# Kernel tuning notes

Hardware: AMD Instinct MI355X
Metric: run time of the kernel (lower is better)

## Reference

```python
import jax, jax.numpy as jnp
import numpy as np

NEG_SLOPE = 0.2
EPS = 1e-16


def gat_conv(x, edge_index, W, a_src, a_dst, b, heads, out_c, concat):
    # PyG GATConv: lin (no bias) -> per-head attention logits -> self-loops ->
    # leaky_relu -> softmax over incoming edges per dst -> weighted scatter-add -> bias
    N = x.shape[0]
    loop = jnp.arange(N)
    src = jnp.concatenate([edge_index[0], loop])  # [E+N]
    dst = jnp.concatenate([edge_index[1], loop])
    h = (x @ W).reshape(N, heads, out_c)                    # [N,H,C]
    a_s = jnp.sum(h * a_src[None], axis=-1)                 # [N,H]
    a_d = jnp.sum(h * a_dst[None], axis=-1)                 # [N,H]
    e = jax.nn.leaky_relu(a_s[src] + a_d[dst], NEG_SLOPE)   # [E+N,H]
    m = jax.ops.segment_max(e, dst, num_segments=N)         # stable softmax per dst
    e = jnp.exp(e - m[dst])
    s = jax.ops.segment_sum(e, dst, num_segments=N)
    alpha = e / (s[dst] + EPS)                              # [E+N,H]
    msg = h[src] * alpha[:, :, None]                        # [E+N,H,C]
    out = jax.ops.segment_sum(msg, dst, num_segments=N)     # [N,H,C]
    out = out.reshape(N, heads * out_c) if concat else out.mean(axis=1)
    return out + b


def setup_inputs() -> dict:
    key = jax.random.key(0)
    ks = jax.random.split(key, 20)
    N, E = 50000, 800000
    IN, HID, H, OUT = 128, 32, 4, 1
    HC = H * HID  # 128
    g = lambda k, shp: jax.random.normal(k, shp, dtype=jnp.float32) * 0.05
    inp = {
        "x": jax.random.normal(ks[0], (N, IN), dtype=jnp.float32),
        "edge_index": jax.random.randint(ks[1], (2, E), 0, N, dtype=jnp.int64),
        "batch": jnp.zeros((N,), dtype=jnp.int64),
        # conv0: GATConv(128 -> 32, heads=4, concat)
        "c0_w": g(ks[2], (IN, HC)), "c0_asrc": g(ks[3], (H, HID)),
        "c0_adst": g(ks[4], (H, HID)), "c0_b": jnp.zeros((HC,), jnp.float32),
        "s0_w": g(ks[5], (HC, IN)), "s0_b": jnp.zeros((HC,), jnp.float32),
        # conv1: GATConv(128 -> 32, heads=4, concat)
        "c1_w": g(ks[6], (HC, HC)), "c1_asrc": g(ks[7], (H, HID)),
        "c1_adst": g(ks[8], (H, HID)), "c1_b": jnp.zeros((HC,), jnp.float32),
        "s1_w": g(ks[9], (HC, HC)), "s1_b": jnp.zeros((HC,), jnp.float32),
        # conv2: GATConv(128 -> 1, heads=1, concat=False)
        "c2_w": g(ks[10], (HC, OUT)), "c2_asrc": g(ks[11], (1, OUT)),
        "c2_adst": g(ks[12], (1, OUT)), "c2_b": jnp.zeros((OUT,), jnp.float32),
        "s2_w": g(ks[13], (OUT, HC)), "s2_b": jnp.zeros((OUT,), jnp.float32),
    }
    return inp


def reference(x, edge_index, batch,
              c0_w, c0_asrc, c0_adst, c0_b, s0_w, s0_b,
              c1_w, c1_asrc, c1_adst, c1_b, s1_w, s1_b,
              c2_w, c2_asrc, c2_adst, c2_b, s2_w, s2_b):
    # layer 0 (dropout is identity in eval mode)
    h = jax.nn.relu(gat_conv(x, edge_index, c0_w, c0_asrc, c0_adst, c0_b, 4, 32, True)
                    + x @ s0_w.T + s0_b)
    # layer 1
    h = jax.nn.relu(gat_conv(h, edge_index, c1_w, c1_asrc, c1_adst, c1_b, 4, 32, True)
                    + h @ s1_w.T + s1_b)
    # output layer: heads=1, concat=False (mean over heads)
    h = (gat_conv(h, edge_index, c2_w, c2_asrc, c2_adst, c2_b, 1, 1, False)
         + h @ s2_w.T + s2_b)
    return jax.nn.sigmoid(h)
```

## Files before the change

### kernel.cpp

```cpp
#include <hip/hip_runtime.h>
#include <math.h>

#define TPB 256

typedef short bf16x8 __attribute__((ext_vector_type(8)));
typedef float f32x4 __attribute__((ext_vector_type(4)));

static __device__ __forceinline__ float lrelu(float x) { return x > 0.f ? x : 0.2f * x; }
static __device__ __forceinline__ unsigned short f2bf(float f) {
  unsigned u = __float_as_uint(f);
  u += 0x7fffu + ((u >> 16) & 1u);
  return (unsigned short)(u >> 16);
}
static __device__ __forceinline__ float bflo(unsigned w) { return __uint_as_float(w << 16); }
static __device__ __forceinline__ float bfhi(unsigned w) { return __uint_as_float(w & 0xffff0000u); }

__global__ void k_hist(const int* __restrict__ dstE, int E, int N, int* __restrict__ deg) {
  int e = blockIdx.x * TPB + threadIdx.x;
  if (e >= E + N) return;
  int d = (e < E) ? dstE[e] : (e - E);
  d = min(max(d, 0), N - 1);
  atomicAdd(&deg[d], 1);
}

__global__ void k_scan1(const int* __restrict__ deg, int N, int* __restrict__ csum) {
  __shared__ int sm[TPB];
  int t = threadIdx.x, i = blockIdx.x * TPB + t;
  sm[t] = (i < N) ? deg[i] : 0;
  __syncthreads();
  for (int off = TPB / 2; off; off >>= 1) {
    if (t < off) sm[t] += sm[t + off];
    __syncthreads();
  }
  if (t == 0) csum[blockIdx.x] = sm[0];
}

__global__ void k_scan2(int* __restrict__ csum, int nch) {
  __shared__ int sm[TPB];
  int t = threadIdx.x;
  int v = (t < nch) ? csum[t] : 0;
  sm[t] = v;
  __syncthreads();
  for (int off = 1; off < TPB; off <<= 1) {
    int add = (t >= off) ? sm[t - off] : 0;
    __syncthreads();
    sm[t] += add;
    __syncthreads();
  }
  if (t < nch) csum[t] = (t == 0) ? 0 : sm[t - 1];
}

__global__ void k_scan3(const int* __restrict__ deg, const int* __restrict__ csum, int N, int total,
                        int* __restrict__ row_ptr, int* __restrict__ cursor) {
  __shared__ int sm[TPB];
  int b = blockIdx.x, t = threadIdx.x, i = b * TPB + t;
  int v = (i < N) ? deg[i] : 0;
  sm[t] = v;
  __syncthreads();
  for (int off = 1; off < TPB; off <<= 1) {
    int add = (t >= off) ? sm[t - off] : 0;
    __syncthreads();
    sm[t] += add;
    __syncthreads();
  }
  if (i < N) {
    int rp = csum[b] + sm[t] - v;
    row_ptr[i] = rp;
    cursor[i] = rp;
  }
  if (i == 0) row_ptr[N] = total;
}

__global__ void k_scatter(const int* __restrict__ srcE, const int* __restrict__ dstE, int E, int N,
                          int* __restrict__ cursor, int* __restrict__ csr_src) {
  int e = blockIdx.x * TPB + threadIdx.x;
  if (e >= E + N) return;
  int s = (e < E) ? srcE[e] : (e - E);
  int d = (e < E) ? dstE[e] : (e - E);
  s = min(max(s, 0), N - 1);
  d = min(max(d, 0), N - 1);
  int pos = atomicAdd(&cursor[d], 1);
  csr_src[pos] = s;
}

__global__ void k_f2b(const float4* __restrict__ in, uint4* __restrict__ out, int n8) {
  int i = blockIdx.x * TPB + threadIdx.x;
  if (i >= n8) return;
  float4 v0 = in[i * 2], v1 = in[i * 2 + 1];
  uint4 o;
  o.x = (unsigned)f2bf(v0.x) | ((unsigned)f2bf(v0.y) << 16);
  o.y = (unsigned)f2bf(v0.z) | ((unsigned)f2bf(v0.w) << 16);
  o.z = (unsigned)f2bf(v1.x) | ((unsigned)f2bf(v1.y) << 16);
  o.w = (unsigned)f2bf(v1.z) | ((unsigned)f2bf(v1.w) << 16);
  out[i] = o;
}

__global__ void k_prep_w(const float* __restrict__ cW, const float* __restrict__ sW,
                         unsigned short* __restrict__ Wb) {
  int j = blockIdx.x;
  int k = threadIdx.x;
  Wb[j * 128 + k] = f2bf((j < 128) ? cW[k * 128 + j] : sW[(j - 128) * 128 + k]);
}

__global__ __launch_bounds__(TPB) void k_gemm_mfma(const unsigned short* __restrict__ Xb,
                                                   const unsigned short* __restrict__ Wb,
                                                   unsigned short* __restrict__ H16, float* __restrict__ Sb,
                                                   int NR) {
  int wid = threadIdx.x >> 6, lane = threadIdx.x & 63;
  int r0 = blockIdx.x * 64;
  int c0 = wid * 64;
  int l15 = lane & 15, lk = lane >> 4;

  f32x4 acc[4][4];
#pragma unroll
  for (int i = 0; i < 4; ++i)
#pragma unroll
    for (int j = 0; j < 4; ++j) acc[i][j] = (f32x4){0.f, 0.f, 0.f, 0.f};

#pragma unroll
  for (int ks = 0; ks < 4; ++ks) {
    bf16x8 a[4], b[4];
#pragma unroll
    for (int rt = 0; rt < 4; ++rt) {
      int row = min(r0 + rt * 16 + l15, NR - 1);
      a[rt] = *(const bf16x8*)(Xb + (size_t)row * 128 + ks * 32 + lk * 8);
    }
#pragma unroll
    for (int ct = 0; ct < 4; ++ct) {
      int col = c0 + ct * 16 + l15;
      b[ct] = *(const bf16x8*)(Wb + (size_t)col * 128 + ks * 32 + lk * 8);
    }
#pragma unroll
    for (int rt = 0; rt < 4; ++rt)
#pragma unroll
      for (int ct = 0; ct < 4; ++ct)
        acc[rt][ct] = __builtin_amdgcn_mfma_f32_16x16x32_bf16(a[rt], b[ct], acc[rt][ct], 0, 0, 0);
  }

  int orow = lk * 4;
#pragma unroll
  for (int rt = 0; rt < 4; ++rt) {
#pragma unroll
    for (int ct = 0; ct < 4; ++ct) {
      int col = c0 + ct * 16 + l15;
#pragma unroll
      for (int r = 0; r < 4; ++r) {
        int row = r0 + rt * 16 + orow + r;
        if (row < NR) {
          float v = acc[rt][ct][r];
          if (col < 128)
            H16[(size_t)row * 128 + col] = f2bf(v);
          else
            Sb[(size_t)row * 128 + (col - 128)] = v;
        }
      }
    }
  }
}

__global__ void k_asad(const unsigned short* __restrict__ H16, const float* __restrict__ asrc,
                       const float* __restrict__ adst, float* __restrict__ a_s, float* __restrict__ a_d, int N) {
  int i = blockIdx.x * TPB + threadIdx.x;
  if (i >= N * 4) return;
  int n = i >> 2, h = i & 3;
  const uint4* hp = (const uint4*)(H16 + (size_t)n * 128 + h * 32);
  const float4* ap = (const float4*)(asrc + h * 32);
  const float4* bp = (const float4*)(adst + h * 32);
  float sa = 0.f, sd = 0.f;
#pragma unroll
  for (int q = 0; q < 4; ++q) {
    uint4 v = hp[q];
    float f0 = bflo(v.x), f1 = bfhi(v.x), f2 = bflo(v.y), f3 = bfhi(v.y);
    float f4 = bflo(v.z), f5 = bfhi(v.z), f6 = bflo(v.w), f7 = bfhi(v.w);
    float4 a0 = ap[q * 2], a1 = ap[q * 2 + 1];
    float4 b0 = bp[q * 2], b1 = bp[q * 2 + 1];
    sa += f0 * a0.x + f1 * a0.y + f2 * a0.z + f3 * a0.w + f4 * a1.x + f5 * a1.y + f6 * a1.z + f7 * a1.w;
    sd += f0 * b0.x + f1 * b0.y + f2 * b0.z + f3 * b0.w + f4 * b1.x + f5 * b1.y + f6 * b1.z + f7 * b1.w;
  }
  a_s[i] = sa;
  a_d[i] = sd;
}

template <bool BF>
__global__ __launch_bounds__(TPB) void k_smax_agg(const int* __restrict__ row_ptr, const int* __restrict__ csr_src,
                                                  const float4* __restrict__ a_s4, const float4* __restrict__ a_d4,
                                                  const unsigned short* __restrict__ H16,
                                                  const float* __restrict__ Sk, const float* __restrict__ cb,
                                                  const float* __restrict__ sb, float4* __restrict__ spill,
                                                  float* __restrict__ XnF, unsigned short* __restrict__ XnB,
                                                  int N) {
  __shared__ int s_src[4][64];
  __shared__ float s_al[4][256];
  int wid = threadIdx.x >> 6;
  int n = blockIdx.x * 4 + wid;
  if (n >= N) return;
  int lane = threadIdx.x & 63;
  int beg = row_ptr[n], end = row_ptr[n + 1];
  int deg = end - beg;
  float4 ad = a_d4[n];
  int h = lane >> 4;
  float acc0 = 0.f, acc1 = 0.f;

  if (deg <= 64) {
    int s_l = 0;
    float4 lg = make_float4(-1e30f, -1e30f, -1e30f, -1e30f);
    if (lane < deg) {
      s_l = csr_src[beg + lane];
      float4 as = a_s4[s_l];
      lg.x = lrelu(as.x + ad.x);
      lg.y = lrelu(as.y + ad.y);
      lg.z = lrelu(as.z + ad.z);
      lg.w = lrelu(as.w + ad.w);
    }
    int maxoff = (deg <= 16) ? 8 : (deg <= 32) ? 16 : 32;
    float4 mx = lg;
    for (int off = 1; off <= maxoff; off <<= 1) {
      mx.x = fmaxf(mx.x, __shfl_xor(mx.x, off));
      mx.y = fmaxf(mx.y, __shfl_xor(mx.y, off));
      mx.z = fmaxf(mx.z, __shfl_xor(mx.z, off));
      mx.w = fmaxf(mx.w, __shfl_xor(mx.w, off));
    }
    float4 pv = make_float4(0.f, 0.f, 0.f, 0.f);
    if (lane < deg) {
      pv.x = __expf(lg.x - mx.x);
      pv.y = __expf(lg.y - mx.y);
      pv.z = __expf(lg.z - mx.z);
      pv.w = __expf(lg.w - mx.w);
    }
    float4 sm = pv;
    for (int off = 1; off <= maxoff; off <<= 1) {
      sm.x += __shfl_xor(sm.x, off);
      sm.y += __shfl_xor(sm.y, off);
      sm.z += __shfl_xor(sm.z, off);
      sm.w += __shfl_xor(sm.w, off);
    }
    pv.x *= 1.f / (sm.x + 1e-16f);
    pv.y *= 1.f / (sm.y + 1e-16f);
    pv.z *= 1.f / (sm.z + 1e-16f);
    pv.w *= 1.f / (sm.w + 1e-16f);
    s_src[wid][lane] = s_l;
    *(float4*)&s_al[wid][lane * 4] = pv;
    __builtin_amdgcn_wave_barrier();

    const unsigned short* Hb = H16 + lane * 2;
    int dpad = (deg + 3) & ~3;
    for (int j = 0; j < dpad; j += 4) {
      int s0 = s_src[wid][j + 0];
      int s1 = s_src[wid][j + 1];
      int s2 = s_src[wid][j + 2];
      int s3 = s_src[wid][j + 3];
      float a0 = s_al[wid][(j + 0) * 4 + h];
      float a1 = s_al[wid][(j + 1) * 4 + h];
      float a2 = s_al[wid][(j + 2) * 4 + h];
      float a3 = s_al[wid][(j + 3) * 4 + h];
      unsigned w0 = *(const unsigned*)(Hb + (size_t)s0 * 128);
      unsigned w1 = *(const unsigned*)(Hb + (size_t)s1 * 128);
      unsigned w2 = *(const unsigned*)(Hb + (size_t)s2 * 128);
      unsigned w3 = *(const unsigned*)(Hb + (size_t)s3 * 128);
      acc0 = fmaf(a0, bflo(w0), acc0);
      acc1 = fmaf(a0, bfhi(w0), acc1);
      acc0 = fmaf(a1, bflo(w1), acc0);
      acc1 = fmaf(a1, bfhi(w1), acc1);
      acc0 = fmaf(a2, bflo(w2), acc0);
      acc1 = fmaf(a2, bfhi(w2), acc1);
      acc0 = fmaf(a3, bflo(w3), acc0);
      acc1 = fmaf(a3, bfhi(w3), acc1);
    }
  } else {
    float4 mx = make_float4(-1e30f, -1e30f, -1e30f, -1e30f);
    for (int p = beg + lane; p < end; p += 64) {
      int s = csr_src[p];
      float4 as = a_s4[s];
      float4 lg;
      lg.x = lrelu(as.x + ad.x);
      lg.y = lrelu(as.y + ad.y);
      lg.z = lrelu(as.z + ad.z);
      lg.w = lrelu(as.w + ad.w);
      spill[p] = lg;
      mx.x = fmaxf(mx.x, lg.x);
      mx.y = fmaxf(mx.y, lg.y);
      mx.z = fmaxf(mx.z, lg.z);
      mx.w = fmaxf(mx.w, lg.w);
    }
#pragma unroll
    for (int off = 32; off; off >>= 1) {
      mx.x = fmaxf(mx.x, __shfl_xor(mx.x, off));
      mx.y = fmaxf(mx.y, __shfl_xor(mx.y, off));
      mx.z = fmaxf(mx.z, __shfl_xor(mx.z, off));
      mx.w = fmaxf(mx.w, __shfl_xor(mx.w, off));
    }
    __threadfence_block();
    float4 sm = make_float4(0.f, 0.f, 0.f, 0.f);
    for (int p = beg + lane; p < end; p += 64) {
      float4 lg = spill[p];
      float4 pv;
      pv.x = __expf(lg.x - mx.x);
      pv.y = __expf(lg.y - mx.y);
      pv.z = __expf(lg.z - mx.z);
      pv.w = __expf(lg.w - mx.w);
      spill[p] = pv;
      sm.x += pv.x;
      sm.y += pv.y;
      sm.z += pv.z;
      sm.w += pv.w;
    }
#pragma unroll
    for (int off = 32; off; off >>= 1) {
      sm.x += __shfl_xor(sm.x, off);
      sm.y += __shfl_xor(sm.y, off);
      sm.z += __shfl_xor(sm.z, off);
      sm.w += __shfl_xor(sm.w, off);
    }
    float4 inv;
    inv.x = 1.f / (sm.x + 1e-16f);
    inv.y = 1.f / (sm.y + 1e-16f);
    inv.z = 1.f / (sm.z + 1e-16f);
    inv.w = 1.f / (sm.w + 1e-16f);
    __threadfence_block();
    const float* af = (const float*)spill;
    for (int p = beg; p < end; ++p) {
      int s = csr_src[p];
      float av = af[(size_t)p * 4 + h] * ((h == 0) ? inv.x : (h == 1) ? inv.y : (h == 2) ? inv.z : inv.w);
      unsigned w = *(const unsigned*)(H16 + (size_t)s * 128 + lane * 2);
      acc0 = fmaf(av, bflo(w), acc0);
      acc1 = fmaf(av, bfhi(w), acc1);
    }
  }

  int c = lane * 2;
  float2 sk = *(const float2*)(Sk + (size_t)n * 128 + c);
  float2 cbv = *(const float2*)(cb + c);
  float2 sbv = *(const float2*)(sb + c);
  float ox = fmaxf(acc0 + cbv.x + sk.x + sbv.x, 0.f);
  float oy = fmaxf(acc1 + cbv.y + sk.y + sbv.y, 0.f);
  if (BF) {
    unsigned pk = (unsigned)f2bf(ox) | ((unsigned)f2bf(oy) << 16);
    *(unsigned*)(XnB + (size_t)n * 128 + c) = pk;
  } else {
    *(float2*)(XnF + (size_t)n * 128 + c) = make_float2(ox, oy);
  }
}

__global__ void k_l2_lin(const float* __restrict__ X, const float* __restrict__ c2w, const float* __restrict__ s2w,
                         const float* __restrict__ c2as, const float* __restrict__ c2ad, float* __restrict__ h2,
                         float* __restrict__ sk2, float* __restrict__ as2, float* __restrict__ ad2, int N) {
  int gid = blockIdx.x * TPB + threadIdx.x;
  int n = gid >> 6;
  int lane = threadIdx.x & 63;
  if (n >= N) return;
  const float* xp = X + (size_t)n * 128;
  float2 xv = *(const float2*)(xp + lane * 2);
  float2 wv = *(const float2*)(c2w + lane * 2);
  float2 sv = *(const float2*)(s2w + lane * 2);
  float dh = xv.x * wv.x + xv.y * wv.y;
  float ds = xv.x * sv.x + xv.y * sv.y;
  for (int off = 32; off; off >>= 1) {
    dh += __shfl_down(dh, off);
    ds += __shfl_down(ds, off);
  }
  if (lane == 0) {
    h2[n] = dh;
    sk2[n] = ds;
    as2[n] = dh * c2as[0];
    ad2[n] = dh * c2ad[0];
  }
}

__global__ __launch_bounds__(TPB) void k_l2_smax_agg(const int* __restrict__ row_ptr, const int* __restrict__ csr_src,
                                                     const float* __restrict__ as2, const float* __restrict__ ad2,
                                                     const float* __restrict__ h2, const float* __restrict__ sk2,
                                                     const float* __restrict__ c2b, const float* __restrict__ s2b,
                                                     float* __restrict__ out, int N) {
  int n = blockIdx.x * 4 + (threadIdx.x >> 6);
  if (n >= N) return;
  int lane = threadIdx.x & 63;
  int beg = row_ptr[n], end = row_ptr[n + 1];
  int deg = end - beg;
  float ad = ad2[n];
  float num = 0.f, den = 0.f;

  if (deg <= 64) {
    float lg = -1e30f, hv = 0.f;
    if (lane < deg) {
      int s = csr_src[beg + lane];
      lg = lrelu(as2[s] + ad);
      hv = h2[s];
    }
    float mx = lg;
#pragma unroll
    for (int off = 32; off; off >>= 1) mx = fmaxf(mx, __shfl_xor(mx, off));
    float pv = (lane < deg) ? __expf(lg - mx) : 0.f;
    num = pv * hv;
    den = pv;
  } else {
    float mx = -1e30f;
    for (int p = beg + lane; p < end; p += 64) mx = fmaxf(mx, lrelu(as2[csr_src[p]] + ad));
#pragma unroll
    for (int off = 32; off; off >>= 1) mx = fmaxf(mx, __shfl_xor(mx, off));
    for (int p = beg + lane; p < end; p += 64) {
      int s = csr_src[p];
      float pv = __expf(lrelu(as2[s] + ad) - mx);
      num += pv * h2[s];
      den += pv;
    }
  }
#pragma unroll
  for (int off = 32; off; off >>= 1) {
    num += __shfl_xor(num, off);
    den += __shfl_xor(den, off);
  }
  if (lane == 0) {
    float v = num / (den + 1e-16f) + c2b[0] + sk2[n] + s2b[0];
    out[n] = 1.f / (1.f + __expf(-v));
  }
}

extern "C" void kernel_launch(void* const* d_in, const int* in_sizes, int n_in,
                              void* d_out, int out_size, void* d_ws, size_t ws_size,
                              hipStream_t stream) {
  const float* x = (const float*)d_in[0];
  const int* ei = (const int*)d_in[1];
  const float* c0_w = (const float*)d_in[3];
  const float* c0_as = (const float*)d_in[4];
  const float* c0_ad = (const float*)d_in[5];
  const float* c0_b = (const float*)d_in[6];
  const float* s0_w = (const float*)d_in[7];
  const float* s0_b = (const float*)d_in[8];
  const float* c1_w = (const float*)d_in[9];
  const float* c1_as = (const float*)d_in[10];
  const float* c1_ad = (const float*)d_in[11];
  const float* c1_b = (const float*)d_in[12];
  const float* s1_w = (const float*)d_in[13];
  const float* s1_b = (const float*)d_in[14];
  const float* c2_w = (const float*)d_in[15];
  const float* c2_as = (const float*)d_in[16];
  const float* c2_ad = (const float*)d_in[17];
  const float* c2_b = (const float*)d_in[18];
  const float* s2_w = (const float*)d_in[19];
  const float* s2_b = (const float*)d_in[20];

  const int N = in_sizes[0] / 128;
  const int E = in_sizes[1] / 2;
  const int EN = E + N;
  const int* srcE = ei;
  const int* dstE = ei + E;

  char* wp_ = (char*)d_ws;
  auto alloc = [&](size_t bytes) -> void* {
    void* r = (void*)wp_;
    wp_ += (bytes + 255) & ~(size_t)255;
    return r;
  };
  unsigned short* Xb0 = (unsigned short*)alloc((size_t)N * 128 * 2);
  unsigned short* Xb1 = (unsigned short*)alloc((size_t)N * 128 * 2);
  unsigned short* H16 = (unsigned short*)alloc((size_t)N * 128 * 2);
  float* Sk = (float*)alloc((size_t)N * 128 * 4);
  float* P2 = (float*)alloc((size_t)N * 128 * 4);
  float* a_s = (float*)alloc((size_t)N * 4 * 4);
  float* a_d = (float*)alloc((size_t)N * 4 * 4);
  float* spill = (float*)alloc((size_t)EN * 4 * 4);
  unsigned short* Wb = (unsigned short*)alloc(256 * 128 * 2);
  int* deg = (int*)alloc((size_t)N * 4);
  int* row_ptr = (int*)alloc((size_t)(N + 1) * 4);
  int* cursor = (int*)alloc((size_t)N * 4);
  int* csum = (int*)alloc(4096 * 4);
  int* csr_src = (int*)alloc((size_t)EN * 4);
  float* h2 = (float*)alloc((size_t)N * 4);
  float* sk2 = (float*)alloc((size_t)N * 4);
  float* as2 = (float*)alloc((size_t)N * 4);
  float* ad2 = (float*)alloc((size_t)N * 4);

  const int gEN = (EN + TPB - 1) / TPB;
  const int gN4 = (N * 4 + TPB - 1) / TPB;
  const int nch = (N + TPB - 1) / TPB;
  const int gGemm = (N + 63) / 64;
  const int gWave = (N + 3) / 4;
  const int n8 = N * 128 / 8;

  hipMemsetAsync(deg, 0, (size_t)N * 4, stream);
  k_hist<<<gEN, TPB, 0, stream>>>(dstE, E, N, deg);
  k_scan1<<<nch, TPB, 0, stream>>>(deg, N, csum);
  k_scan2<<<1, TPB, 0, stream>>>(csum, nch);
  k_scan3<<<nch, TPB, 0, stream>>>(deg, csum, N, EN, row_ptr, cursor);
  k_scatter<<<gEN, TPB, 0, stream>>>(srcE, dstE, E, N, cursor, csr_src);

  k_f2b<<<(n8 + TPB - 1) / TPB, TPB, 0, stream>>>((const float4*)x, (uint4*)Xb0, n8);
  k_prep_w<<<256, 128, 0, stream>>>(c0_w, s0_w, Wb);
  k_gemm_mfma<<<gGemm, TPB, 0, stream>>>(Xb0, Wb, H16, Sk, N);
  k_asad<<<gN4, TPB, 0, stream>>>(H16, c0_as, c0_ad, a_s, a_d, N);
  k_smax_agg<true><<<gWave, TPB, 0, stream>>>(row_ptr, csr_src, (const float4*)a_s, (const float4*)a_d, H16, Sk,
                                              c0_b, s0_b, (float4*)spill, nullptr, Xb1, N);

  k_prep_w<<<256, 128, 0, stream>>>(c1_w, s1_w, Wb);
  k_gemm_mfma<<<gGemm, TPB, 0, stream>>>(Xb1, Wb, H16, Sk, N);
  k_asad<<<gN4, TPB, 0, stream>>>(H16, c1_as, c1_ad, a_s, a_d, N);
  k_smax_agg<false><<<gWave, TPB, 0, stream>>>(row_ptr, csr_src, (const float4*)a_s, (const float4*)a_d, H16, Sk,
                                               c1_b, s1_b, (float4*)spill, P2, nullptr, N);

  k_l2_lin<<<(N * 64 + TPB - 1) / TPB, TPB, 0, stream>>>(P2, c2_w, s2_w, c2_as, c2_ad, h2, sk2, as2, ad2, N);
  k_l2_smax_agg<<<gWave, TPB, 0, stream>>>(row_ptr, csr_src, as2, ad2, h2, sk2, c2_b, s2_b, (float*)d_out, N);
}
```

Measured before the change: 388.4 us.

## Split aggregation by head slice, partition CSR build by destination range, bf16 skip

```diff
diff --git a/kernel.cpp b/kernel.cpp
--- a/kernel.cpp
+++ b/kernel.cpp
@@ -2,6 +2,7 @@
 #include <math.h>
 
 #define TPB 256
+#define RB 128
 
 typedef short bf16x8 __attribute__((ext_vector_type(8)));
 typedef float f32x4 __attribute__((ext_vector_type(4)));
@@ -15,12 +16,16 @@
 static __device__ __forceinline__ float bflo(unsigned w) { return __uint_as_float(w << 16); }
 static __device__ __forceinline__ float bfhi(unsigned w) { return __uint_as_float(w & 0xffff0000u); }
 
-__global__ void k_hist(const int* __restrict__ dstE, int E, int N, int* __restrict__ deg) {
-  int e = blockIdx.x * TPB + threadIdx.x;
-  if (e >= E + N) return;
-  int d = (e < E) ? dstE[e] : (e - E);
-  d = min(max(d, 0), N - 1);
-  atomicAdd(&deg[d], 1);
+__global__ void k_hist8(const int* __restrict__ dstE, int E, int N, int* __restrict__ deg) {
+  int r = blockIdx.x & 7;
+  int nb = gridDim.x >> 3;
+  int lo = (int)(((long)r * N) / 8), hi = (int)(((long)(r + 1) * N) / 8);
+  int EN = E + N;
+  for (int e = (blockIdx.x >> 3) * TPB + threadIdx.x; e < EN; e += nb * TPB) {
+    int d = (e < E) ? dstE[e] : (e - E);
+    d = min(max(d, 0), N - 1);
+    if (d >= lo && d < hi) atomicAdd(&deg[d], 1);
+  }
 }
 
 __global__ void k_scan1(const int* __restrict__ deg, int N, int* __restrict__ csum) {
@@ -71,16 +76,22 @@
   if (i == 0) row_ptr[N] = total;
 }
 
-__global__ void k_scatter(const int* __restrict__ srcE, const int* __restrict__ dstE, int E, int N,
-                          int* __restrict__ cursor, int* __restrict__ csr_src) {
-  int e = blockIdx.x * TPB + threadIdx.x;
-  if (e >= E + N) return;
-  int s = (e < E) ? srcE[e] : (e - E);
-  int d = (e < E) ? dstE[e] : (e - E);
-  s = min(max(s, 0), N - 1);
-  d = min(max(d, 0), N - 1);
-  int pos = atomicAdd(&cursor[d], 1);
-  csr_src[pos] = s;
+__global__ void k_scatter8(const int* __restrict__ srcE, const int* __restrict__ dstE, int E, int N,
+                           int* __restrict__ cursor, int* __restrict__ csr_src) {
+  int r = blockIdx.x & 7;
+  int nb = gridDim.x >> 3;
+  int lo = (int)(((long)r * N) / 8), hi = (int)(((long)(r + 1) * N) / 8);
+  int EN = E + N;
+  for (int e = (blockIdx.x >> 3) * TPB + threadIdx.x; e < EN; e += nb * TPB) {
+    int d = (e < E) ? dstE[e] : (e - E);
+    d = min(max(d, 0), N - 1);
+    if (d >= lo && d < hi) {
+      int s = (e < E) ? srcE[e] : (e - E);
+      s = min(max(s, 0), N - 1);
+      int pos = atomicAdd(&cursor[d], 1);
+      csr_src[pos] = s;
+    }
+  }
 }
 
 __global__ void k_f2b(const float4* __restrict__ in, uint4* __restrict__ out, int n8) {
@@ -95,17 +106,22 @@
   out[i] = o;
 }
 
-__global__ void k_prep_w(const float* __restrict__ cW, const float* __restrict__ sW,
-                         unsigned short* __restrict__ Wb) {
-  int j = blockIdx.x;
+__global__ void k_prep_w2(const float* __restrict__ cW0, const float* __restrict__ sW0,
+                          const float* __restrict__ cW1, const float* __restrict__ sW1,
+                          unsigned short* __restrict__ Wb0, unsigned short* __restrict__ Wb1) {
+  int j = blockIdx.x & 255;
+  int which = blockIdx.x >> 8;
   int k = threadIdx.x;
+  const float* cW = which ? cW1 : cW0;
+  const float* sW = which ? sW1 : sW0;
+  unsigned short* Wb = which ? Wb1 : Wb0;
   Wb[j * 128 + k] = f2bf((j < 128) ? cW[k * 128 + j] : sW[(j - 128) * 128 + k]);
 }
 
 __global__ __launch_bounds__(TPB) void k_gemm_mfma(const unsigned short* __restrict__ Xb,
                                                    const unsigned short* __restrict__ Wb,
-                                                   unsigned short* __restrict__ H16, float* __restrict__ Sb,
-                                                   int NR) {
+                                                   unsigned short* __restrict__ H16,
+                                                   unsigned short* __restrict__ Sk16, int NR) {
   int wid = threadIdx.x >> 6, lane = threadIdx.x & 63;
   int r0 = blockIdx.x * 64;
   int c0 = wid * 64;
@@ -151,7 +167,7 @@
           if (col < 128)
             H16[(size_t)row * 128 + col] = f2bf(v);
           else
-            Sb[(size_t)row * 128 + (col - 128)] = v;
+            Sk16[(size_t)row * 128 + (col - 128)] = f2bf(v);
         }
       }
     }
@@ -183,161 +199,104 @@
 
 template <bool BF>
 __global__ __launch_bounds__(TPB) void k_smax_agg(const int* __restrict__ row_ptr, const int* __restrict__ csr_src,
-                                                  const float4* __restrict__ a_s4, const float4* __restrict__ a_d4,
+                                                  const float* __restrict__ a_s, const float* __restrict__ a_d,
                                                   const unsigned short* __restrict__ H16,
-                                                  const float* __restrict__ Sk, const float* __restrict__ cb,
-                                                  const float* __restrict__ sb, float4* __restrict__ spill,
-                                                  float* __restrict__ XnF, unsigned short* __restrict__ XnB,
-                                                  int N) {
+                                                  const unsigned short* __restrict__ Sk16,
+                                                  const float* __restrict__ cb, const float* __restrict__ sb,
+                                                  float* __restrict__ spill, float* __restrict__ XnF,
+                                                  unsigned short* __restrict__ XnB, int N) {
   __shared__ int s_src[4][64];
-  __shared__ float s_al[4][256];
+  __shared__ float s_al[4][64];
+  int b = blockIdx.x;
+  int s = (b & 7) >> 1;
+  int q = ((b >> 3) << 1) + (b & 1);
   int wid = threadIdx.x >> 6;
-  int n = blockIdx.x * 4 + wid;
+  int n = q * 4 + wid;
   if (n >= N) return;
   int lane = threadIdx.x & 63;
+  int eg = lane >> 4, cl = lane & 15;
+  int c = s * 32 + cl * 2;
   int beg = row_ptr[n], end = row_ptr[n + 1];
   int deg = end - beg;
-  float4 ad = a_d4[n];
-  int h = lane >> 4;
+  float ad = a_d[n * 4 + s];
   float acc0 = 0.f, acc1 = 0.f;
 
   if (deg <= 64) {
     int s_l = 0;
-    float4 lg = make_float4(-1e30f, -1e30f, -1e30f, -1e30f);
+    float lg = -1e30f;
     if (lane < deg) {
       s_l = csr_src[beg + lane];
-      float4 as = a_s4[s_l];
-      lg.x = lrelu(as.x + ad.x);
-      lg.y = lrelu(as.y + ad.y);
-      lg.z = lrelu(as.z + ad.z);
-      lg.w = lrelu(as.w + ad.w);
+      lg = lrelu(a_s[s_l * 4 + s] + ad);
     }
     int maxoff = (deg <= 16) ? 8 : (deg <= 32) ? 16 : 32;
-    float4 mx = lg;
-    for (int off = 1; off <= maxoff; off <<= 1) {
-      mx.x = fmaxf(mx.x, __shfl_xor(mx.x, off));
-      mx.y = fmaxf(mx.y, __shfl_xor(mx.y, off));
-      mx.z = fmaxf(mx.z, __shfl_xor(mx.z, off));
-      mx.w = fmaxf(mx.w, __shfl_xor(mx.w, off));
-    }
-    float4 pv = make_float4(0.f, 0.f, 0.f, 0.f);
-    if (lane < deg) {
-      pv.x = __expf(lg.x - mx.x);
-      pv.y = __expf(lg.y - mx.y);
-      pv.z = __expf(lg.z - mx.z);
-      pv.w = __expf(lg.w - mx.w);
-    }
-    float4 sm = pv;
-    for (int off = 1; off <= maxoff; off <<= 1) {
-      sm.x += __shfl_xor(sm.x, off);
-      sm.y += __shfl_xor(sm.y, off);
-      sm.z += __shfl_xor(sm.z, off);
-      sm.w += __shfl_xor(sm.w, off);
-    }
-    pv.x *= 1.f / (sm.x + 1e-16f);
-    pv.y *= 1.f / (sm.y + 1e-16f);
-    pv.z *= 1.f / (sm.z + 1e-16f);
-    pv.w *= 1.f / (sm.w + 1e-16f);
+    float mx = lg;
+    for (int off = 1; off <= maxoff; off <<= 1) mx = fmaxf(mx, __shfl_xor(mx, off));
+    float pv = (lane < deg) ? __expf(lg - mx) : 0.f;
+    float sm = pv;
+    for (int off = 1; off <= maxoff; off <<= 1) sm += __shfl_xor(sm, off);
+    pv *= 1.f / (sm + 1e-16f);
     s_src[wid][lane] = s_l;
-    *(float4*)&s_al[wid][lane * 4] = pv;
+    s_al[wid][lane] = pv;
     __builtin_amdgcn_wave_barrier();
 
-    const unsigned short* Hb = H16 + lane * 2;
+    const unsigned short* Hb = H16 + c;
     int dpad = (deg + 3) & ~3;
     for (int j = 0; j < dpad; j += 4) {
-      int s0 = s_src[wid][j + 0];
-      int s1 = s_src[wid][j + 1];
-      int s2 = s_src[wid][j + 2];
-      int s3 = s_src[wid][j + 3];
-      float a0 = s_al[wid][(j + 0) * 4 + h];
-      float a1 = s_al[wid][(j + 1) * 4 + h];
-      float a2 = s_al[wid][(j + 2) * 4 + h];
-      float a3 = s_al[wid][(j + 3) * 4 + h];
-      unsigned w0 = *(const unsigned*)(Hb + (size_t)s0 * 128);
-      unsigned w1 = *(const unsigned*)(Hb + (size_t)s1 * 128);
-      unsigned w2 = *(const unsigned*)(Hb + (size_t)s2 * 128);
-      unsigned w3 = *(const unsigned*)(Hb + (size_t)s3 * 128);
-      acc0 = fmaf(a0, bflo(w0), acc0);
-      acc1 = fmaf(a0, bfhi(w0), acc1);
-      acc0 = fmaf(a1, bflo(w1), acc0);
-      acc1 = fmaf(a1, bfhi(w1), acc1);
-      acc0 = fmaf(a2, bflo(w2), acc0);
-      acc1 = fmaf(a2, bfhi(w2), acc1);
-      acc0 = fmaf(a3, bflo(w3), acc0);
-      acc1 = fmaf(a3, bfhi(w3), acc1);
+      int sj = s_src[wid][j + eg];
+      float aj = s_al[wid][j + eg];
+      unsigned w = *(const unsigned*)(Hb + (size_t)sj * 128);
+      acc0 = fmaf(aj, bflo(w), acc0);
+      acc1 = fmaf(aj, bfhi(w), acc1);
     }
   } else {
-    float4 mx = make_float4(-1e30f, -1e30f, -1e30f, -1e30f);
+    float mx = -1e30f;
     for (int p = beg + lane; p < end; p += 64) {
-      int s = csr_src[p];
-      float4 as = a_s4[s];
-      float4 lg;
-      lg.x = lrelu(as.x + ad.x);
-      lg.y = lrelu(as.y + ad.y);
-      lg.z = lrelu(as.z + ad.z);
-      lg.w = lrelu(as.w + ad.w);
-      spill[p] = lg;
-      mx.x = fmaxf(mx.x, lg.x);
-      mx.y = fmaxf(mx.y, lg.y);
-      mx.z = fmaxf(mx.z, lg.z);
-      mx.w = fmaxf(mx.w, lg.w);
-    }
-#pragma unroll
-    for (int off = 32; off; off >>= 1) {
-      mx.x = fmaxf(mx.x, __shfl_xor(mx.x, off));
-      mx.y = fmaxf(mx.y, __shfl_xor(mx.y, off));
-      mx.z = fmaxf(mx.z, __shfl_xor(mx.z, off));
-      mx.w = fmaxf(mx.w, __shfl_xor(mx.w, off));
-    }
+      float lg = lrelu(a_s[csr_src[p] * 4 + s] + ad);
+      spill[(size_t)p * 4 + s] = lg;
+      mx = fmaxf(mx, lg);
+    }
+#pragma unroll
+    for (int off = 32; off; off >>= 1) mx = fmaxf(mx, __shfl_xor(mx, off));
     __threadfence_block();
-    float4 sm = make_float4(0.f, 0.f, 0.f, 0.f);
+    float sm = 0.f;
     for (int p = beg + lane; p < end; p += 64) {
-      float4 lg = spill[p];
-      float4 pv;
-      pv.x = __expf(lg.x - mx.x);
-      pv.y = __expf(lg.y - mx.y);
-      pv.z = __expf(lg.z - mx.z);
-      pv.w = __expf(lg.w - mx.w);
-      spill[p] = pv;
-      sm.x += pv.x;
-      sm.y += pv.y;
-      sm.z += pv.z;
-      sm.w += pv.w;
-    }
-#pragma unroll
-    for (int off = 32; off; off >>= 1) {
-      sm.x += __shfl_xor(sm.x, off);
-      sm.y += __shfl_xor(sm.y, off);
-      sm.z += __shfl_xor(sm.z, off);
-      sm.w += __shfl_xor(sm.w, off);
-    }
-    float4 inv;
-    inv.x = 1.f / (sm.x + 1e-16f);
-    inv.y = 1.f / (sm.y + 1e-16f);
-    inv.z = 1.f / (sm.z + 1e-16f);
-    inv.w = 1.f / (sm.w + 1e-16f);
+      float pv = __expf(spill[(size_t)p * 4 + s] - mx);
+      spill[(size_t)p * 4 + s] = pv;
+      sm += pv;
+    }
+#pragma unroll
+    for (int off = 32; off; off >>= 1) sm += __shfl_xor(sm, off);
+    float inv = 1.f / (sm + 1e-16f);
     __threadfence_block();
-    const float* af = (const float*)spill;
-    for (int p = beg; p < end; ++p) {
-      int s = csr_src[p];
-      float av = af[(size_t)p * 4 + h] * ((h == 0) ? inv.x : (h == 1) ? inv.y : (h == 2) ? inv.z : inv.w);
-      unsigned w = *(const unsigned*)(H16 + (size_t)s * 128 + lane * 2);
-      acc0 = fmaf(av, bflo(w), acc0);
-      acc1 = fmaf(av, bfhi(w), acc1);
-    }
-  }
-
-  int c = lane * 2;
-  float2 sk = *(const float2*)(Sk + (size_t)n * 128 + c);
-  float2 cbv = *(const float2*)(cb + c);
-  float2 sbv = *(const float2*)(sb + c);
-  float ox = fmaxf(acc0 + cbv.x + sk.x + sbv.x, 0.f);
-  float oy = fmaxf(acc1 + cbv.y + sk.y + sbv.y, 0.f);
-  if (BF) {
-    unsigned pk = (unsigned)f2bf(ox) | ((unsigned)f2bf(oy) << 16);
-    *(unsigned*)(XnB + (size_t)n * 128 + c) = pk;
-  } else {
-    *(float2*)(XnF + (size_t)n * 128 + c) = make_float2(ox, oy);
+    for (int j = 0; j < deg; j += 4) {
+      int p = beg + j + eg;
+      if (p < end) {
+        int sj = csr_src[p];
+        float aj = spill[(size_t)p * 4 + s] * inv;
+        unsigned w = *(const unsigned*)(H16 + (size_t)sj * 128 + c);
+        acc0 = fmaf(aj, bflo(w), acc0);
+        acc1 = fmaf(aj, bfhi(w), acc1);
+      }
+    }
+  }
+
+  acc0 += __shfl_xor(acc0, 16);
+  acc0 += __shfl_xor(acc0, 32);
+  acc1 += __shfl_xor(acc1, 16);
+  acc1 += __shfl_xor(acc1, 32);
+
+  if (eg == 0) {
+    unsigned skw = *(const unsigned*)(Sk16 + (size_t)n * 128 + c);
+    float2 cbv = *(const float2*)(cb + c);
+    float2 sbv = *(const float2*)(sb + c);
+    float ox = fmaxf(acc0 + cbv.x + bflo(skw) + sbv.x, 0.f);
+    float oy = fmaxf(acc1 + cbv.y + bfhi(skw) + sbv.y, 0.f);
+    if (BF) {
+      unsigned pk = (unsigned)f2bf(ox) | ((unsigned)f2bf(oy) << 16);
+      *(unsigned*)(XnB + (size_t)n * 128 + c) = pk;
+    } else {
+      *(float2*)(XnF + (size_t)n * 128 + c) = make_float2(ox, oy);
+    }
   }
 }
 
@@ -454,12 +413,13 @@
   unsigned short* Xb0 = (unsigned short*)alloc((size_t)N * 128 * 2);
   unsigned short* Xb1 = (unsigned short*)alloc((size_t)N * 128 * 2);
   unsigned short* H16 = (unsigned short*)alloc((size_t)N * 128 * 2);
-  float* Sk = (float*)alloc((size_t)N * 128 * 4);
+  unsigned short* Sk16 = (unsigned short*)alloc((size_t)N * 128 * 2);
   float* P2 = (float*)alloc((size_t)N * 128 * 4);
   float* a_s = (float*)alloc((size_t)N * 4 * 4);
   float* a_d = (float*)alloc((size_t)N * 4 * 4);
   float* spill = (float*)alloc((size_t)EN * 4 * 4);
-  unsigned short* Wb = (unsigned short*)alloc(256 * 128 * 2);
+  unsigned short* Wb0 = (unsigned short*)alloc(256 * 128 * 2);
+  unsigned short* Wb1 = (unsigned short*)alloc(256 * 128 * 2);
   int* deg = (int*)alloc((size_t)N * 4);
   int* row_ptr = (int*)alloc((size_t)(N + 1) * 4);
   int* cursor = (int*)alloc((size_t)N * 4);
@@ -470,32 +430,32 @@
   float* as2 = (float*)alloc((size_t)N * 4);
   float* ad2 = (float*)alloc((size_t)N * 4);
 
-  const int gEN = (EN + TPB - 1) / TPB;
   const int gN4 = (N * 4 + TPB - 1) / TPB;
   const int nch = (N + TPB - 1) / TPB;
   const int gGemm = (N + 63) / 64;
   const int gWave = (N + 3) / 4;
+  const int gSlice = ((N + 7) / 8) * 8;
   const int n8 = N * 128 / 8;
 
   hipMemsetAsync(deg, 0, (size_t)N * 4, stream);
-  k_hist<<<gEN, TPB, 0, stream>>>(dstE, E, N, deg);
+  k_hist8<<<8 * RB, TPB, 0, stream>>>(dstE, E, N, deg);
   k_scan1<<<nch, TPB, 0, stream>>>(deg, N, csum);
   k_scan2<<<1, TPB, 0, stream>>>(csum, nch);
   k_scan3<<<nch, TPB, 0, stream>>>(deg, csum, N, EN, row_ptr, cursor);
-  k_scatter<<<gEN, TPB, 0, stream>>>(srcE, dstE, E, N, cursor, csr_src);
+  k_scatter8<<<8 * RB, TPB, 0, stream>>>(srcE, dstE, E, N, cursor, csr_src);
 
   k_f2b<<<(n8 + TPB - 1) / TPB, TPB, 0, stream>>>((const float4*)x, (uint4*)Xb0, n8);
-  k_prep_w<<<256, 128, 0, stream>>>(c0_w, s0_w, Wb);
-  k_gemm_mfma<<<gGemm, TPB, 0, stream>>>(Xb0, Wb, H16, Sk, N);
+  k_prep_w2<<<512, 128, 0, stream>>>(c0_w, s0_w, c1_w, s1_w, Wb0, Wb1);
+
+  k_gemm_mfma<<<gGemm, TPB, 0, stream>>>(Xb0, Wb0, H16, Sk16, N);
   k_asad<<<gN4, TPB, 0, stream>>>(H16, c0_as, c0_ad, a_s, a_d, N);
-  k_smax_agg<true><<<gWave, TPB, 0, stream>>>(row_ptr, csr_src, (const float4*)a_s, (const float4*)a_d, H16, Sk,
-                                              c0_b, s0_b, (float4*)spill, nullptr, Xb1, N);
-
-  k_prep_w<<<256, 128, 0, stream>>>(c1_w, s1_w, Wb);
-  k_gemm_mfma<<<gGemm, TPB, 0, stream>>>(Xb1, Wb, H16, Sk, N);
+  k_smax_agg<true><<<gSlice, TPB, 0, stream>>>(row_ptr, csr_src, a_s, a_d, H16, Sk16, c0_b, s0_b, spill, nullptr,
+                                               Xb1, N);
+
+  k_gemm_mfma<<<gGemm, TPB, 0, stream>>>(Xb1, Wb1, H16, Sk16, N);
   k_asad<<<gN4, TPB, 0, stream>>>(H16, c1_as, c1_ad, a_s, a_d, N);
-  k_smax_agg<false><<<gWave, TPB, 0, stream>>>(row_ptr, csr_src, (const float4*)a_s, (const float4*)a_d, H16, Sk,
-                                               c1_b, s1_b, (float4*)spill, P2, nullptr, N);
+  k_smax_agg<false><<<gSlice, TPB, 0, stream>>>(row_ptr, csr_src, a_s, a_d, H16, Sk16, c1_b, s1_b, spill, P2,
+                                                nullptr, N);
 
   k_l2_lin<<<(N * 64 + TPB - 1) / TPB, TPB, 0, stream>>>(P2, c2_w, s2_w, c2_as, c2_ad, h2, sk2, as2, ad2, N);
   k_l2_smax_agg<<<gWave, TPB, 0, stream>>>(row_ptr, csr_src, as2, ad2, h2, sk2, c2_b, s2_b, (float*)d_out, N);
```

After: 509.9 us. +31.3%, slower.
